# Performance work log

Hardware: AMD Instinct MI355X
Metric: run time of the kernel (lower is better)

The kernel has to match this reference:

```python
import jax, jax.numpy as jnp
import numpy as np

B, S, D, H, E, K = 2, 1024, 1024, 2048, 8, 2


def setup_inputs() -> dict:
    key = jax.random.key(0)
    k1, k2, k3, k4 = jax.random.split(key, 4)
    x = jax.random.normal(k1, (B, S, D), dtype=jnp.float32)
    # router initialized to zeros in the module; use small random weights so
    # top-k routing is non-degenerate for a correctness baseline
    router_w = 0.02 * jax.random.normal(k2, (E, D), dtype=jnp.float32)
    router_b = jnp.zeros((E,), dtype=jnp.float32)
    w12 = 0.02 * jax.random.normal(k3, (E, D, 2 * H), dtype=jnp.float32)
    w3 = 0.02 * jax.random.normal(k4, (E, H, D), dtype=jnp.float32)
    return {"x": x, "router_w": router_w, "router_b": router_b, "w12": w12, "w3": w3}


def reference(x, router_w, router_b, w12, w3):
    # Router (eval mode: no jitter noise)
    logits = jnp.einsum("bsd,ed->bse", x, router_w) + router_b      # [B,S,E]
    scores = jax.nn.sigmoid(logits)
    top_vals, top_idx = jax.lax.top_k(scores, K)                     # [B,S,K]
    rweights = top_vals / (jnp.sum(top_vals, axis=-1, keepdims=True) + 1e-6)
    # per-expert combine weight: sum over top-k slots where idx == e
    onehot = jax.nn.one_hot(top_idx, E, dtype=x.dtype)               # [B,S,K,E]
    combine = jnp.einsum("bsk,bske->bse", rweights, onehot)          # [B,S,E]
    # Dense per-expert SwiGLU over all tokens (matches naive module math)
    h12 = jnp.einsum("bsd,edh->ebsh", x, w12)                        # [E,B,S,2H]
    h1, h2 = jnp.split(h12, 2, axis=-1)
    hidden = jax.nn.silu(h1) * h2                                    # [E,B,S,H]
    expert_out = jnp.einsum("ebsh,ehd->ebsd", hidden, w3)            # [E,B,S,D]
    out = jnp.einsum("ebsd,bse->bsd", expert_out, combine)           # [B,S,D]
    aux_loss = 0.01 * jnp.mean(logits ** 2)
    return out, aux_loss
```

## Files before the change

kernel.cpp:

```cpp
#include <hip/hip_runtime.h>
#include <math.h>
#include <stdint.h>

#define B_ 2
#define S_ 1024
#define D_ 1024
#define H_ 2048
#define E_ 8
#define TOK_ (B_*S_)
#define N1_ (2*H_)
#define PAIRS_ (TOK_*2)

typedef float f32x4 __attribute__((ext_vector_type(4)));
typedef short short8 __attribute__((ext_vector_type(8)));

__device__ __forceinline__ unsigned short f2bf(float f) {
  unsigned int u = __float_as_uint(f);
  u += 0x7fffu + ((u >> 16) & 1u);
  return (unsigned short)(u >> 16);
}

__global__ __launch_bounds__(256) void transpose_f32_to_bf16(
    const float* __restrict__ src, unsigned short* __restrict__ dst, int R, int C)
{
  __shared__ float tile[64][65];
  const int e = blockIdx.z;
  const float* s = src + (size_t)e * R * C;
  unsigned short* d = dst + (size_t)e * R * C;
  const int c0 = blockIdx.x * 64, r0 = blockIdx.y * 64;
  const int tx = threadIdx.x & 63;
  const int ty = threadIdx.x >> 6;
#pragma unroll
  for (int i = 0; i < 16; ++i) {
    int r = ty + i * 4;
    tile[r][tx] = s[(size_t)(r0 + r) * C + c0 + tx];
  }
  __syncthreads();
#pragma unroll
  for (int i = 0; i < 16; ++i) {
    int c = ty + i * 4;
    d[(size_t)(c0 + c) * R + r0 + tx] = f2bf(tile[tx][c]);
  }
}

__global__ __launch_bounds__(256) void router_kernel(
    const float* __restrict__ x, const float* __restrict__ rw,
    const float* __restrict__ rb, int* __restrict__ counts,
    int* __restrict__ expert_of, int* __restrict__ slot_of,
    float* __restrict__ w_of, float* __restrict__ tok_ssq)
{
  const int wave = threadIdx.x >> 6, lane = threadIdx.x & 63;
  const int t = blockIdx.x * 4 + wave;
  const float* xr = x + (size_t)t * D_;
  float acc[E_];
#pragma unroll
  for (int e = 0; e < E_; ++e) acc[e] = 0.f;
  for (int d = lane; d < D_; d += 64) {
    float xv = xr[d];
#pragma unroll
    for (int e = 0; e < E_; ++e) acc[e] += xv * rw[e * D_ + d];
  }
#pragma unroll
  for (int e = 0; e < E_; ++e) {
    float v = acc[e];
#pragma unroll
    for (int sh = 32; sh > 0; sh >>= 1) v += __shfl_xor(v, sh, 64);
    acc[e] = v;
  }
  if (lane == 0) {
    float logits[E_], sc[E_], ssq = 0.f;
#pragma unroll
    for (int e = 0; e < E_; ++e) {
      logits[e] = acc[e] + rb[e];
      ssq += logits[e] * logits[e];
      sc[e] = 1.f / (1.f + __expf(-logits[e]));
    }
    tok_ssq[t] = ssq;
    int i1 = 0;
#pragma unroll
    for (int e = 1; e < E_; ++e) if (sc[e] > sc[i1]) i1 = e;
    int i2 = (i1 == 0) ? 1 : 0;
#pragma unroll
    for (int e = 0; e < E_; ++e)
      if (e != i1 && e != i2 && sc[e] > sc[i2]) i2 = e;
    float v1 = sc[i1], v2 = sc[i2];
    float inv = 1.f / (v1 + v2 + 1e-6f);
    int s1 = atomicAdd(&counts[i1], 1);
    int s2 = atomicAdd(&counts[i2], 1);
    expert_of[t * 2]     = i1; slot_of[t * 2]     = s1; w_of[t * 2]     = v1 * inv;
    expert_of[t * 2 + 1] = i2; slot_of[t * 2 + 1] = s2; w_of[t * 2 + 1] = v2 * inv;
  }
}

__global__ void offsets_kernel(const int* __restrict__ counts, int* __restrict__ offsets)
{
  if (threadIdx.x == 0) {
    int o = 0;
    for (int e = 0; e < E_; ++e) { offsets[e] = o; o += counts[e]; }
  }
}

__global__ __launch_bounds__(256) void aux_kernel(const float* __restrict__ tok_ssq,
                                                  float* __restrict__ out_aux)
{
  __shared__ float sm[256];
  float s = 0.f;
  for (int i = threadIdx.x; i < TOK_; i += 256) s += tok_ssq[i];
  sm[threadIdx.x] = s;
  __syncthreads();
  for (int h = 128; h > 0; h >>= 1) {
    if (threadIdx.x < h) sm[threadIdx.x] += sm[threadIdx.x + h];
    __syncthreads();
  }
  if (threadIdx.x == 0) *out_aux = 0.01f * sm[0] / (float)(TOK_ * E_);
}

__global__ __launch_bounds__(256) void pack_kernel(
    const float* __restrict__ x, const int* __restrict__ expert_of,
    const int* __restrict__ slot_of, const float* __restrict__ w_of,
    const int* __restrict__ offsets, unsigned short* __restrict__ px,
    int* __restrict__ tok_ids, float* __restrict__ tok_w)
{
  const int pair = blockIdx.x;
  const int t = pair >> 1;
  const int e = expert_of[pair];
  const int row = offsets[e] + slot_of[pair];
  if (threadIdx.x == 0) { tok_ids[row] = t; tok_w[row] = w_of[pair]; }
  const float4* xr = (const float4*)(x + (size_t)t * D_);
  ushort4* pr = (ushort4*)(px + (size_t)row * D_);
  float4 v = xr[threadIdx.x];
  ushort4 o;
  o.x = f2bf(v.x); o.y = f2bf(v.y); o.z = f2bf(v.z); o.w = f2bf(v.w);
  pr[threadIdx.x] = o;
}

__device__ __forceinline__ void stage_tile(const unsigned short* gbase, int gstride,
                                           unsigned short* sbase, int kk,
                                           int wave, int lane)
{
#pragma unroll
  for (int c = 0; c < 2; ++c) {
    const unsigned short* g = gbase
        + (size_t)(wave * 32 + c * 16 + (lane >> 2)) * gstride + kk + (lane & 3) * 8;
    unsigned short* s = sbase + (wave * 32 + c * 16) * 32;
    __builtin_amdgcn_global_load_lds(
        (const __attribute__((address_space(1))) void*)g,
        (__attribute__((address_space(3))) void*)s, 16, 0, 0);
  }
}

__global__ __launch_bounds__(256, 2) void gemm1_kernel(
    const unsigned short* __restrict__ px, const unsigned short* __restrict__ w12t,
    unsigned short* __restrict__ hid, const int* __restrict__ counts,
    const int* __restrict__ offsets)
{
  const int e = blockIdx.z, mt = blockIdx.y, nt = blockIdx.x;
  const int cnt = counts[e];
  if (mt * 128 >= cnt) return;
  const int off = offsets[e];
  const int tid = threadIdx.x;
  const int wave = tid >> 6, lane = tid & 63;
  const int wm = wave >> 1, wn = wave & 1;
  const int lr = lane & 15, lk = lane >> 4;

  __shared__ __align__(16) unsigned short As[128 * 32];
  __shared__ __align__(16) unsigned short B1s[128 * 32];
  __shared__ __align__(16) unsigned short B2s[128 * 32];

  f32x4 zero = {0.f, 0.f, 0.f, 0.f};
  f32x4 acc1[4][4], acc2[4][4];
#pragma unroll
  for (int mi = 0; mi < 4; ++mi)
#pragma unroll
    for (int ni = 0; ni < 4; ++ni) { acc1[mi][ni] = zero; acc2[mi][ni] = zero; }

  const unsigned short* Abase  = px + (size_t)(off + mt * 128) * D_;
  const unsigned short* B1base = w12t + ((size_t)e * N1_ + nt * 128) * D_;
  const unsigned short* B2base = w12t + ((size_t)e * N1_ + H_ + nt * 128) * D_;

  for (int kk = 0; kk < D_; kk += 32) {
    stage_tile(Abase, D_, As, kk, wave, lane);
    stage_tile(B1base, D_, B1s, kk, wave, lane);
    stage_tile(B2base, D_, B2s, kk, wave, lane);
    __syncthreads();
    short8 a[4], b1[4], b2[4];
#pragma unroll
    for (int i = 0; i < 4; ++i) {
      a[i]  = *(const short8*)&As[(wm * 64 + i * 16 + lr) * 32 + lk * 8];
      b1[i] = *(const short8*)&B1s[(wn * 64 + i * 16 + lr) * 32 + lk * 8];
      b2[i] = *(const short8*)&B2s[(wn * 64 + i * 16 + lr) * 32 + lk * 8];
    }
#pragma unroll
    for (int mi = 0; mi < 4; ++mi)
#pragma unroll
      for (int ni = 0; ni < 4; ++ni) {
        acc1[mi][ni] = __builtin_amdgcn_mfma_f32_16x16x32_bf16(a[mi], b1[ni], acc1[mi][ni], 0, 0, 0);
        acc2[mi][ni] = __builtin_amdgcn_mfma_f32_16x16x32_bf16(a[mi], b2[ni], acc2[mi][ni], 0, 0, 0);
      }
    __syncthreads();
  }

#pragma unroll
  for (int mi = 0; mi < 4; ++mi)
#pragma unroll
    for (int r = 0; r < 4; ++r) {
      int row_local = mt * 128 + wm * 64 + mi * 16 + lk * 4 + r;
      if (row_local < cnt) {
#pragma unroll
        for (int ni = 0; ni < 4; ++ni) {
          int col = nt * 128 + wn * 64 + ni * 16 + lr;
          float v1 = acc1[mi][ni][r];
          float v2 = acc2[mi][ni][r];
          float hval = (v1 / (1.f + __expf(-v1))) * v2;
          hid[(size_t)(off + row_local) * H_ + col] = f2bf(hval);
        }
      }
    }
}

__global__ __launch_bounds__(256, 2) void gemm2_kernel(
    const unsigned short* __restrict__ hid, const unsigned short* __restrict__ w3t,
    const int* __restrict__ counts, const int* __restrict__ offsets,
    const int* __restrict__ tok_ids, const float* __restrict__ tok_w,
    float* __restrict__ out)
{
  const int e = blockIdx.z, mt = blockIdx.y, nt = blockIdx.x;
  const int cnt = counts[e];
  if (mt * 128 >= cnt) return;
  const int off = offsets[e];
  const int tid = threadIdx.x;
  const int wave = tid >> 6, lane = tid & 63;
  const int wm = wave >> 1, wn = wave & 1;
  const int lr = lane & 15, lk = lane >> 4;

  __shared__ __align__(16) unsigned short As[128 * 32];
  __shared__ __align__(16) unsigned short Bs[128 * 32];

  f32x4 zero = {0.f, 0.f, 0.f, 0.f};
  f32x4 acc[4][4];
#pragma unroll
  for (int mi = 0; mi < 4; ++mi)
#pragma unroll
    for (int ni = 0; ni < 4; ++ni) acc[mi][ni] = zero;

  const unsigned short* Abase = hid + (size_t)(off + mt * 128) * H_;
  const unsigned short* Bbase = w3t + ((size_t)e * D_ + nt * 128) * H_;

  for (int kk = 0; kk < H_; kk += 32) {
    stage_tile(Abase, H_, As, kk, wave, lane);
    stage_tile(Bbase, H_, Bs, kk, wave, lane);
    __syncthreads();
    short8 a[4], b[4];
#pragma unroll
    for (int i = 0; i < 4; ++i) {
      a[i] = *(const short8*)&As[(wm * 64 + i * 16 + lr) * 32 + lk * 8];
      b[i] = *(const short8*)&Bs[(wn * 64 + i * 16 + lr) * 32 + lk * 8];
    }
#pragma unroll
    for (int mi = 0; mi < 4; ++mi)
#pragma unroll
      for (int ni = 0; ni < 4; ++ni)
        acc[mi][ni] = __builtin_amdgcn_mfma_f32_16x16x32_bf16(a[mi], b[ni], acc[mi][ni], 0, 0, 0);
    __syncthreads();
  }

#pragma unroll
  for (int mi = 0; mi < 4; ++mi)
#pragma unroll
    for (int r = 0; r < 4; ++r) {
      int row_local = mt * 128 + wm * 64 + mi * 16 + lk * 4 + r;
      if (row_local < cnt) {
        int g = off + row_local;
        int t = tok_ids[g];
        float wgt = tok_w[g];
#pragma unroll
        for (int ni = 0; ni < 4; ++ni) {
          int col = nt * 128 + wn * 64 + ni * 16 + lr;
          atomicAdd(&out[(size_t)t * D_ + col], acc[mi][ni][r] * wgt);
        }
      }
    }
}

extern "C" void kernel_launch(void* const* d_in, const int* in_sizes, int n_in,
                              void* d_out, int out_size, void* d_ws, size_t ws_size,
                              hipStream_t stream)
{
  const float* x   = (const float*)d_in[0];
  const float* rw  = (const float*)d_in[1];
  const float* rb  = (const float*)d_in[2];
  const float* w12 = (const float*)d_in[3];
  const float* w3  = (const float*)d_in[4];
  float* out = (float*)d_out;

  char* wsb = (char*)d_ws;
  int*   counts    = (int*)(wsb + 0);
  int*   offsets   = (int*)(wsb + 64);
  int*   expert_of = (int*)(wsb + 1024);
  int*   slot_of   = (int*)(wsb + 1024 + 16384);
  float* w_of      = (float*)(wsb + 1024 + 2 * 16384);
  int*   tok_ids   = (int*)(wsb + 1024 + 3 * 16384);
  float* tok_w     = (float*)(wsb + 1024 + 4 * 16384);
  float* tok_ssq   = (float*)(wsb + 1024 + 5 * 16384);
  unsigned short* px   = (unsigned short*)(wsb + (128 << 10));
  unsigned short* hid  = (unsigned short*)(wsb + (128 << 10) + ((size_t)8  << 20));
  unsigned short* w12t = (unsigned short*)(wsb + (128 << 10) + ((size_t)24 << 20));
  unsigned short* w3t  = (unsigned short*)(wsb + (128 << 10) + ((size_t)88 << 20));

  hipMemsetAsync(counts, 0, E_ * sizeof(int), stream);
  hipMemsetAsync(out, 0, (size_t)out_size * sizeof(float), stream);

  transpose_f32_to_bf16<<<dim3(N1_ / 64, D_ / 64, E_), 256, 0, stream>>>(w12, w12t, D_, N1_);
  transpose_f32_to_bf16<<<dim3(D_ / 64, H_ / 64, E_), 256, 0, stream>>>(w3, w3t, H_, D_);
  router_kernel<<<TOK_ / 4, 256, 0, stream>>>(x, rw, rb, counts, expert_of, slot_of, w_of, tok_ssq);
  offsets_kernel<<<1, 64, 0, stream>>>(counts, offsets);
  aux_kernel<<<1, 256, 0, stream>>>(tok_ssq, out + (size_t)TOK_ * D_);
  pack_kernel<<<PAIRS_, 256, 0, stream>>>(x, expert_of, slot_of, w_of, offsets, px, tok_ids, tok_w);
  gemm1_kernel<<<dim3(16, 16, 8), 256, 0, stream>>>(px, w12t, hid, counts, offsets);
  gemm2_kernel<<<dim3(8, 16, 8), 256, 0, stream>>>(hid, w3t, counts, offsets, tok_ids, tok_w, out);
}
```

Measured before the change: 489.1 us.

## Compact MoE tile list, split-K gemm2, swizzle LDS, vectorize transpose and router

Builds a compact per-expert tile list in offsets_kernel so the grouped GEMMs launch only over real 128-row tiles instead of a padded 16x8 grid. Gemm2 is split along K into two halves that both accumulate into the output atomically, and its occupancy bound is raised to 4. Shared-memory fragments are XOR-swizzled to cut bank conflicts. The weight transpose now writes ushort2 pairs and the router reads float4. The costs are doubled atomic traffic in gemm2 and clamped redundant row loads for partial tiles.

New measurement: 445.7 us. 1.1x faster.

```diff
diff --git a/kernel.cpp b/kernel.cpp
--- a/kernel.cpp
+++ b/kernel.cpp
@@ -10,6 +10,7 @@
 #define TOK_ (B_*S_)
 #define N1_ (2*H_)
 #define PAIRS_ (TOK_*2)
+#define MAXTILES_ 40
 
 typedef float f32x4 __attribute__((ext_vector_type(4)));
 typedef short short8 __attribute__((ext_vector_type(8)));
@@ -36,10 +37,15 @@
     tile[r][tx] = s[(size_t)(r0 + r) * C + c0 + tx];
   }
   __syncthreads();
-#pragma unroll
-  for (int i = 0; i < 16; ++i) {
-    int c = ty + i * 4;
-    d[(size_t)(c0 + c) * R + r0 + tx] = f2bf(tile[tx][c]);
+  const int rx = (threadIdx.x & 31) * 2;
+  const int cy = threadIdx.x >> 5;
+#pragma unroll
+  for (int i = 0; i < 8; ++i) {
+    int c = cy + i * 8;
+    ushort2 o;
+    o.x = f2bf(tile[rx][c]);
+    o.y = f2bf(tile[rx + 1][c]);
+    *(ushort2*)&d[(size_t)(c0 + c) * R + r0 + rx] = o;
   }
 }
 
@@ -51,14 +57,20 @@
 {
   const int wave = threadIdx.x >> 6, lane = threadIdx.x & 63;
   const int t = blockIdx.x * 4 + wave;
-  const float* xr = x + (size_t)t * D_;
+  const float4* x4 = (const float4*)(x + (size_t)t * D_);
+  const float4* rw4 = (const float4*)rw;
   float acc[E_];
 #pragma unroll
   for (int e = 0; e < E_; ++e) acc[e] = 0.f;
-  for (int d = lane; d < D_; d += 64) {
-    float xv = xr[d];
-#pragma unroll
-    for (int e = 0; e < E_; ++e) acc[e] += xv * rw[e * D_ + d];
+#pragma unroll
+  for (int d4 = 0; d4 < D_ / 4 / 64; ++d4) {
+    int idx = d4 * 64 + lane;
+    float4 xv = x4[idx];
+#pragma unroll
+    for (int e = 0; e < E_; ++e) {
+      float4 wv = rw4[e * (D_ / 4) + idx];
+      acc[e] += xv.x * wv.x + xv.y * wv.y + xv.z * wv.z + xv.w * wv.w;
+    }
   }
 #pragma unroll
   for (int e = 0; e < E_; ++e) {
@@ -92,11 +104,19 @@
   }
 }
 
-__global__ void offsets_kernel(const int* __restrict__ counts, int* __restrict__ offsets)
+__global__ void offsets_kernel(const int* __restrict__ counts, int* __restrict__ offsets,
+                               int* __restrict__ tile_e, int* __restrict__ tile_m0)
 {
   if (threadIdx.x == 0) {
-    int o = 0;
-    for (int e = 0; e < E_; ++e) { offsets[e] = o; o += counts[e]; }
+    int o = 0, nt = 0;
+    for (int e = 0; e < E_; ++e) {
+      offsets[e] = o;
+      for (int m0 = 0; m0 < counts[e]; m0 += 128) {
+        tile_e[nt] = e; tile_m0[nt] = m0; ++nt;
+      }
+      o += counts[e];
+    }
+    for (; nt < MAXTILES_; ++nt) tile_e[nt] = -1;
   }
 }
 
@@ -138,10 +158,11 @@
                                            unsigned short* sbase, int kk,
                                            int wave, int lane)
 {
+  const int seg = (lane & 3) ^ ((lane >> 3) & 3);
 #pragma unroll
   for (int c = 0; c < 2; ++c) {
     const unsigned short* g = gbase
-        + (size_t)(wave * 32 + c * 16 + (lane >> 2)) * gstride + kk + (lane & 3) * 8;
+        + (size_t)(wave * 32 + c * 16 + (lane >> 2)) * gstride + kk + seg * 8;
     unsigned short* s = sbase + (wave * 32 + c * 16) * 32;
     __builtin_amdgcn_global_load_lds(
         (const __attribute__((address_space(1))) void*)g,
@@ -149,14 +170,40 @@
   }
 }
 
+__device__ __forceinline__ void stage_tile_clamped(const unsigned short* gbase, int gstride,
+                                                   int row0, int rowmax,
+                                                   unsigned short* sbase, int kk,
+                                                   int wave, int lane)
+{
+  const int seg = (lane & 3) ^ ((lane >> 3) & 3);
+#pragma unroll
+  for (int c = 0; c < 2; ++c) {
+    int r = row0 + wave * 32 + c * 16 + (lane >> 2);
+    r = (r < rowmax) ? r : rowmax - 1;
+    const unsigned short* g = gbase + (size_t)r * gstride + kk + seg * 8;
+    unsigned short* s = sbase + (wave * 32 + c * 16) * 32;
+    __builtin_amdgcn_global_load_lds(
+        (const __attribute__((address_space(1))) void*)g,
+        (__attribute__((address_space(3))) void*)s, 16, 0, 0);
+  }
+}
+
+__device__ __forceinline__ short8 read_frag(const unsigned short* smem, int row, int lk) {
+  const int s = lk ^ ((row >> 1) & 3);
+  return *(const short8*)&smem[row * 32 + s * 8];
+}
+
 __global__ __launch_bounds__(256, 2) void gemm1_kernel(
     const unsigned short* __restrict__ px, const unsigned short* __restrict__ w12t,
     unsigned short* __restrict__ hid, const int* __restrict__ counts,
-    const int* __restrict__ offsets)
-{
-  const int e = blockIdx.z, mt = blockIdx.y, nt = blockIdx.x;
+    const int* __restrict__ offsets, const int* __restrict__ tile_e,
+    const int* __restrict__ tile_m0)
+{
+  const int ti = blockIdx.y, nt = blockIdx.x;
+  const int e = tile_e[ti];
+  if (e < 0) return;
+  const int m0 = tile_m0[ti];
   const int cnt = counts[e];
-  if (mt * 128 >= cnt) return;
   const int off = offsets[e];
   const int tid = threadIdx.x;
   const int wave = tid >> 6, lane = tid & 63;
@@ -174,21 +221,20 @@
 #pragma unroll
     for (int ni = 0; ni < 4; ++ni) { acc1[mi][ni] = zero; acc2[mi][ni] = zero; }
 
-  const unsigned short* Abase  = px + (size_t)(off + mt * 128) * D_;
   const unsigned short* B1base = w12t + ((size_t)e * N1_ + nt * 128) * D_;
   const unsigned short* B2base = w12t + ((size_t)e * N1_ + H_ + nt * 128) * D_;
 
   for (int kk = 0; kk < D_; kk += 32) {
-    stage_tile(Abase, D_, As, kk, wave, lane);
+    stage_tile_clamped(px, D_, off + m0, PAIRS_, As, kk, wave, lane);
     stage_tile(B1base, D_, B1s, kk, wave, lane);
     stage_tile(B2base, D_, B2s, kk, wave, lane);
     __syncthreads();
     short8 a[4], b1[4], b2[4];
 #pragma unroll
     for (int i = 0; i < 4; ++i) {
-      a[i]  = *(const short8*)&As[(wm * 64 + i * 16 + lr) * 32 + lk * 8];
-      b1[i] = *(const short8*)&B1s[(wn * 64 + i * 16 + lr) * 32 + lk * 8];
-      b2[i] = *(const short8*)&B2s[(wn * 64 + i * 16 + lr) * 32 + lk * 8];
+      a[i]  = read_frag(As,  wm * 64 + i * 16 + lr, lk);
+      b1[i] = read_frag(B1s, wn * 64 + i * 16 + lr, lk);
+      b2[i] = read_frag(B2s, wn * 64 + i * 16 + lr, lk);
     }
 #pragma unroll
     for (int mi = 0; mi < 4; ++mi)
@@ -204,7 +250,7 @@
   for (int mi = 0; mi < 4; ++mi)
 #pragma unroll
     for (int r = 0; r < 4; ++r) {
-      int row_local = mt * 128 + wm * 64 + mi * 16 + lk * 4 + r;
+      int row_local = m0 + wm * 64 + mi * 16 + lk * 4 + r;
       if (row_local < cnt) {
 #pragma unroll
         for (int ni = 0; ni < 4; ++ni) {
@@ -218,15 +264,18 @@
     }
 }
 
-__global__ __launch_bounds__(256, 2) void gemm2_kernel(
+__global__ __launch_bounds__(256, 4) void gemm2_kernel(
     const unsigned short* __restrict__ hid, const unsigned short* __restrict__ w3t,
     const int* __restrict__ counts, const int* __restrict__ offsets,
+    const int* __restrict__ tile_e, const int* __restrict__ tile_m0,
     const int* __restrict__ tok_ids, const float* __restrict__ tok_w,
     float* __restrict__ out)
 {
-  const int e = blockIdx.z, mt = blockIdx.y, nt = blockIdx.x;
+  const int ti = blockIdx.y, nt = blockIdx.x, ks = blockIdx.z;
+  const int e = tile_e[ti];
+  if (e < 0) return;
+  const int m0 = tile_m0[ti];
   const int cnt = counts[e];
-  if (mt * 128 >= cnt) return;
   const int off = offsets[e];
   const int tid = threadIdx.x;
   const int wave = tid >> 6, lane = tid & 63;
@@ -243,18 +292,18 @@
 #pragma unroll
     for (int ni = 0; ni < 4; ++ni) acc[mi][ni] = zero;
 
-  const unsigned short* Abase = hid + (size_t)(off + mt * 128) * H_;
   const unsigned short* Bbase = w3t + ((size_t)e * D_ + nt * 128) * H_;
 
-  for (int kk = 0; kk < H_; kk += 32) {
-    stage_tile(Abase, H_, As, kk, wave, lane);
+  const int k0 = ks * (H_ / 2), k1 = k0 + (H_ / 2);
+  for (int kk = k0; kk < k1; kk += 32) {
+    stage_tile_clamped(hid, H_, off + m0, PAIRS_, As, kk, wave, lane);
     stage_tile(Bbase, H_, Bs, kk, wave, lane);
     __syncthreads();
     short8 a[4], b[4];
 #pragma unroll
     for (int i = 0; i < 4; ++i) {
-      a[i] = *(const short8*)&As[(wm * 64 + i * 16 + lr) * 32 + lk * 8];
-      b[i] = *(const short8*)&Bs[(wn * 64 + i * 16 + lr) * 32 + lk * 8];
+      a[i] = read_frag(As, wm * 64 + i * 16 + lr, lk);
+      b[i] = read_frag(Bs, wn * 64 + i * 16 + lr, lk);
     }
 #pragma unroll
     for (int mi = 0; mi < 4; ++mi)
@@ -268,7 +317,7 @@
   for (int mi = 0; mi < 4; ++mi)
 #pragma unroll
     for (int r = 0; r < 4; ++r) {
-      int row_local = mt * 128 + wm * 64 + mi * 16 + lk * 4 + r;
+      int row_local = m0 + wm * 64 + mi * 16 + lk * 4 + r;
       if (row_local < cnt) {
         int g = off + row_local;
         int t = tok_ids[g];
@@ -296,6 +345,8 @@
   char* wsb = (char*)d_ws;
   int*   counts    = (int*)(wsb + 0);
   int*   offsets   = (int*)(wsb + 64);
+  int*   tile_e    = (int*)(wsb + 128);
+  int*   tile_m0   = (int*)(wsb + 384);
   int*   expert_of = (int*)(wsb + 1024);
   int*   slot_of   = (int*)(wsb + 1024 + 16384);
   float* w_of      = (float*)(wsb + 1024 + 2 * 16384);
@@ -313,9 +364,9 @@
   transpose_f32_to_bf16<<<dim3(N1_ / 64, D_ / 64, E_), 256, 0, stream>>>(w12, w12t, D_, N1_);
   transpose_f32_to_bf16<<<dim3(D_ / 64, H_ / 64, E_), 256, 0, stream>>>(w3, w3t, H_, D_);
   router_kernel<<<TOK_ / 4, 256, 0, stream>>>(x, rw, rb, counts, expert_of, slot_of, w_of, tok_ssq);
-  offsets_kernel<<<1, 64, 0, stream>>>(counts, offsets);
+  offsets_kernel<<<1, 64, 0, stream>>>(counts, offsets, tile_e, tile_m0);
   aux_kernel<<<1, 256, 0, stream>>>(tok_ssq, out + (size_t)TOK_ * D_);
   pack_kernel<<<PAIRS_, 256, 0, stream>>>(x, expert_of, slot_of, w_of, offsets, px, tok_ids, tok_w);
-  gemm1_kernel<<<dim3(16, 16, 8), 256, 0, stream>>>(px, w12t, hid, counts, offsets);
-  gemm2_kernel<<<dim3(8, 16, 8), 256, 0, stream>>>(hid, w3t, counts, offsets, tok_ids, tok_w, out);
-}
+  gemm1_kernel<<<dim3(16, MAXTILES_), 256, 0, stream>>>(px, w12t, hid, counts, offsets, tile_e, tile_m0);
+  gemm2_kernel<<<dim3(8, MAXTILES_, 2), 256, 0, stream>>>(hid, w3t, counts, offsets, tile_e, tile_m0, tok_ids, tok_w, out);
+}
```
